# Kernel tuning notes

Hardware: AMD Instinct MI355X
Metric: run time of the kernel (lower is better)

The kernel has to match this reference:

```python
import jax, jax.numpy as jnp
import numpy as np

N_HEADS = 16
LATENT = 16          # latent_vec_len (1D RoPE portion of head_dim)
ROPE_BASE = 10000.0
HIDDEN = 1024


def _rope_1d_tables(seq_len, d):
    m = d // 2
    inv_freq = 1.0 / (ROPE_BASE ** (jnp.arange(m, dtype=jnp.float32) * 2.0 / d))
    ang = jnp.arange(seq_len, dtype=jnp.float32)[:, None] * inv_freq[None, :]  # (S, m)
    return jnp.cos(ang), jnp.sin(ang)


def _rope_2d_tables(height, width, d):
    m = d // 4
    inv_freq = 1.0 / (ROPE_BASE ** (jnp.arange(m, dtype=jnp.float32) * 4.0 / d))
    xa = jnp.arange(width, dtype=jnp.float32)[:, None] * inv_freq[None, :]   # (W, m)
    ya = jnp.arange(height, dtype=jnp.float32)[:, None] * inv_freq[None, :]  # (H, m)
    S = height * width
    cos_x = jnp.broadcast_to(jnp.cos(xa)[None, :, :], (height, width, m)).reshape(S, m)
    sin_x = jnp.broadcast_to(jnp.sin(xa)[None, :, :], (height, width, m)).reshape(S, m)
    cos_y = jnp.broadcast_to(jnp.cos(ya)[:, None, :], (height, width, m)).reshape(S, m)
    sin_y = jnp.broadcast_to(jnp.sin(ya)[:, None, :], (height, width, m)).reshape(S, m)
    return cos_x, sin_x, cos_y, sin_y


def _apply_rope_1d(x, cos, sin):
    # x: (B, n, S, d) with d even; cos/sin: (S, d//2)
    d = x.shape[-1]
    xr = x.reshape(*x.shape[:-1], d // 2, 2)
    a, b = xr[..., 0], xr[..., 1]
    na = a * cos - b * sin
    nb = a * sin + b * cos
    return jnp.stack((na, nb), axis=-1).reshape(x.shape)


def _apply_rope_2d(x, cos_x, sin_x, cos_y, sin_y):
    # x: (B, n, S, d) with d % 4 == 0; tables: (S, d//4)
    q = x.shape[-1] // 4
    xr, xi = x[..., :q], x[..., q:2 * q]
    yr, yi = x[..., 2 * q:3 * q], x[..., 3 * q:]
    return jnp.concatenate([
        xr * cos_x - xi * sin_x,
        xr * sin_x + xi * cos_x,
        yr * cos_y - yi * sin_y,
        yr * sin_y + yi * cos_y,
    ], axis=-1)


def setup_inputs() -> dict:
    key = jax.random.key(0)
    ks = jax.random.split(key, 9)
    B, S, D = 16, 1024, HIDDEN
    s = 1.0 / np.sqrt(D)
    inp = {
        'x': jax.random.normal(ks[0], (B, S, D), dtype=jnp.float32),
        'Wq': jax.random.uniform(ks[1], (D, D), jnp.float32, -s, s),
        'bq': jax.random.uniform(ks[2], (D,), jnp.float32, -s, s),
        'Wk': jax.random.uniform(ks[3], (D, D), jnp.float32, -s, s),
        'bk': jax.random.uniform(ks[4], (D,), jnp.float32, -s, s),
        'Wv': jax.random.uniform(ks[5], (D, D), jnp.float32, -s, s),
        'bv': jax.random.uniform(ks[6], (D,), jnp.float32, -s, s),
        'Wo': jax.random.uniform(ks[7], (D, D), jnp.float32, -s, s),
        'bo': jax.random.uniform(ks[8], (D,), jnp.float32, -s, s),
        'height': 32,
        'width': 32,
    }
    return inp


def reference(x, Wq, bq, Wk, bk, Wv, bv, Wo, bo, height, width):
    B, S, D = x.shape
    n, h = N_HEADS, D // N_HEADS
    spatial = h - LATENT
    scale = 1.0 / np.sqrt(h)

    def heads(t):
        return t.reshape(B, S, n, h).transpose(0, 2, 1, 3)  # (B, n, S, h)

    q = heads(x @ Wq.T + bq)
    k = heads(x @ Wk.T + bk)
    v = heads(x @ Wv.T + bv)

    cos1, sin1 = _rope_1d_tables(S, LATENT)
    cx, sx, cy, sy = _rope_2d_tables(height, width, spatial)

    ql = _apply_rope_1d(q[..., :LATENT], cos1, sin1)
    kl = _apply_rope_1d(k[..., :LATENT], cos1, sin1)
    qs = _apply_rope_2d(q[..., LATENT:], cx, sx, cy, sy)
    ks_ = _apply_rope_2d(k[..., LATENT:], cx, sx, cy, sy)

    qr = jnp.concatenate([ql, qs], axis=-1)
    kr = jnp.concatenate([kl, ks_], axis=-1)

    attn = jax.nn.softmax(jnp.einsum('bnsh,bnth->bnst', qr, kr) * scale, axis=-1)
    out = jnp.einsum('bnst,bnth->bnsh', attn, v)
    out = out.transpose(0, 2, 1, 3).reshape(B, S, D)
    return out @ Wo.T + bo
```

## Files before the change

### kernel.cpp

```cpp
#include <hip/hip_runtime.h>
#include <math.h>

#define B_ 16
#define S_ 1024
#define D_ 1024
#define NH_ 16
#define M_TOT (B_ * S_)

typedef __attribute__((ext_vector_type(8))) short short8v;
typedef __attribute__((ext_vector_type(4))) short short4v;
typedef __attribute__((ext_vector_type(4))) float float4v;
typedef __attribute__((ext_vector_type(4))) unsigned int uint4v;

static __device__ __forceinline__ unsigned short f2bf(float f) {
  union { float f; unsigned u; } x; x.f = f;
  unsigned r = (x.u + 0x7fffu + ((x.u >> 16) & 1u)) >> 16;
  return (unsigned short)r;
}
static __device__ __forceinline__ float bf2f(unsigned short u) {
  union { unsigned u; float f; } x; x.u = ((unsigned)u) << 16;
  return x.f;
}

static __device__ __forceinline__ unsigned pack2bf(float a, float b) {
  return ((unsigned)f2bf(b) << 16) | (unsigned)f2bf(a);
}

static __device__ __forceinline__ void load_lds16(const unsigned short* g, unsigned short* l) {
  __builtin_amdgcn_global_load_lds(
      (const __attribute__((address_space(1))) unsigned int*)g,
      (__attribute__((address_space(3))) unsigned int*)l, 16, 0, 0);
}

__global__ void build_tables(float* __restrict__ cos1, float* __restrict__ sin1,
                             float* __restrict__ cos2, float* __restrict__ sin2) {
  int t = blockIdx.x * 256 + threadIdx.x;
  if (t < S_ * 8) {
    int s = t >> 3, i = t & 7;
    double ang = (double)s * pow(10000.0, -(double)i / 8.0);
    cos1[t] = (float)cos(ang);
    sin1[t] = (float)sin(ang);
  } else if (t < S_ * 8 + 384) {
    int u = t - S_ * 8;
    int p = u / 12, j = u - p * 12;
    double ang = (double)p * pow(10000.0, -(double)j / 12.0);
    cos2[u] = (float)cos(ang);
    sin2[u] = (float)sin(ang);
  }
}

__global__ __launch_bounds__(256) void f32_to_bf16(
    const float* __restrict__ src, unsigned short* __restrict__ dst, int n4) {
  int i = blockIdx.x * 256 + threadIdx.x;
  if (i < n4) {
    float4 v = ((const float4*)src)[i];
    unsigned short t[4] = {f2bf(v.x), f2bf(v.y), f2bf(v.z), f2bf(v.w)};
    ((short4v*)dst)[i] = *(short4v*)t;
  }
}

__global__ __launch_bounds__(256) void w4_to_bf16(
    const float* __restrict__ w0, const float* __restrict__ w1,
    const float* __restrict__ w2, const float* __restrict__ w3,
    unsigned short* __restrict__ dst) {
  const float* srcs[4] = {w0, w1, w2, w3};
  const float* src = srcs[blockIdx.y];
  unsigned short* d = dst + (size_t)blockIdx.y * D_ * D_;
  int i = blockIdx.x * 256 + threadIdx.x;
  float4 v = ((const float4*)src)[i];
  unsigned short t[4] = {f2bf(v.x), f2bf(v.y), f2bf(v.z), f2bf(v.w)};
  ((short4v*)d)[i] = *(short4v*)t;
}

template <bool BF16OUT>
__global__ __launch_bounds__(256) void gemm_mfma(
    const unsigned short* __restrict__ A, const unsigned short* __restrict__ W,
    const float* __restrict__ bias, void* __restrict__ Cout) {
  __shared__ unsigned short As[128 * 32];
  __shared__ unsigned short Bs[128 * 32];
  const int t = threadIdx.x;
  const int w = t >> 6, L = t & 63;
  const int c = L & 15, g = L >> 4;
  const int id = blockIdx.x;
  const int xcd = id & 7, slot = id >> 3;
  const int bn = (slot & 7) * 128;
  const int bm = ((slot >> 3) * 8 + xcd) * 128;

  const int srow = w * 32 + (L >> 2);
  const int sko = (L & 3) * 8;
  const unsigned short* gA = A + (size_t)(bm + srow) * D_ + sko;
  const unsigned short* gB = W + (size_t)(bn + srow) * D_ + sko;
  unsigned short* lA = As + w * 1024;
  unsigned short* lB = Bs + w * 1024;

  const int wm = (w >> 1) * 64, wn = (w & 1) * 64;

  float4v acc[4][4];
#pragma unroll
  for (int i = 0; i < 4; ++i)
#pragma unroll
    for (int j = 0; j < 4; ++j) acc[i][j] = (float4v){0.f, 0.f, 0.f, 0.f};

  for (int k0 = 0; k0 < D_; k0 += 32) {
    __syncthreads();
    load_lds16(gA + k0, lA);
    load_lds16(gA + k0 + 16 * D_, lA + 512);
    load_lds16(gB + k0, lB);
    load_lds16(gB + k0 + 16 * D_, lB + 512);
    __syncthreads();
    short8v af[4], bf[4];
#pragma unroll
    for (int i = 0; i < 4; ++i)
      af[i] = *(const short8v*)&As[(wm + 16 * i + c) * 32 + 8 * g];
#pragma unroll
    for (int j = 0; j < 4; ++j)
      bf[j] = *(const short8v*)&Bs[(wn + 16 * j + c) * 32 + 8 * g];
#pragma unroll
    for (int i = 0; i < 4; ++i)
#pragma unroll
      for (int j = 0; j < 4; ++j)
        acc[i][j] = __builtin_amdgcn_mfma_f32_16x16x32_bf16(af[i], bf[j], acc[i][j], 0, 0, 0);
  }
#pragma unroll
  for (int i = 0; i < 4; ++i)
#pragma unroll
    for (int r = 0; r < 4; ++r) {
      const size_t row = (size_t)bm + wm + 16 * i + 4 * g + r;
#pragma unroll
      for (int j = 0; j < 4; ++j) {
        const int col = bn + wn + 16 * j + c;
        float vv = acc[i][j][r] + bias[col];
        if (BF16OUT)
          ((unsigned short*)Cout)[row * D_ + col] = f2bf(vv);
        else
          ((float*)Cout)[row * D_ + col] = vv;
      }
    }
}

__global__ __launch_bounds__(256) void rope_inplace(
    unsigned short* q,
    const float* __restrict__ cos1, const float* __restrict__ sin1,
    const float* __restrict__ cos2, const float* __restrict__ sin2,
    float scale) {
  int tid = blockIdx.x * 256 + threadIdx.x;
  int u = tid & 511;
  int m = tid >> 9;
  int s = m & (S_ - 1);
  int head = u >> 5, w = u & 31;
  size_t base = (size_t)m * D_ + head * 64;
  size_t c0, c1;
  float cv, sv;
  if (w < 8) {
    c0 = base + 2 * w; c1 = c0 + 1;
    cv = cos1[s * 8 + w]; sv = sin1[s * 8 + w];
  } else if (w < 20) {
    int j = w - 8, x = s & 31;
    c0 = base + 16 + j; c1 = base + 28 + j;
    cv = cos2[x * 12 + j]; sv = sin2[x * 12 + j];
  } else {
    int j = w - 20, y = s >> 5;
    c0 = base + 40 + j; c1 = base + 52 + j;
    cv = cos2[y * 12 + j]; sv = sin2[y * 12 + j];
  }
  float a = bf2f(q[c0]), b = bf2f(q[c1]);
  q[c0] = f2bf((a * cv - b * sv) * scale);
  q[c1] = f2bf((a * sv + b * cv) * scale);
}

__global__ __launch_bounds__(256) void v_transpose(
    const unsigned short* __restrict__ v, unsigned short* __restrict__ vT) {
  __shared__ unsigned short T[64][72];
  const int t = threadIdx.x;
  const int st0 = blockIdx.x * 64;
  const int hd = blockIdx.y, b = blockIdx.z;
  const unsigned short* src = v + ((size_t)b * S_ + st0) * D_ + hd * 64;
#pragma unroll
  for (int rep = 0; rep < 4; ++rep) {
    int id = t + rep * 256;
    int s = id >> 4, n4 = (id & 15) * 4;
    short4v val = *(const short4v*)(src + (size_t)s * D_ + n4);
    T[n4 + 0][s] = val[0]; T[n4 + 1][s] = val[1];
    T[n4 + 2][s] = val[2]; T[n4 + 3][s] = val[3];
  }
  __syncthreads();
  unsigned short* dst = vT + ((size_t)(b * NH_ + hd) * 64) * S_ + st0;
#pragma unroll
  for (int rep = 0; rep < 2; ++rep) {
    int id = t + rep * 256;
    int n = id >> 3, s8 = (id & 7) * 8;
    unsigned short tmp[8];
#pragma unroll
    for (int u2 = 0; u2 < 8; ++u2) tmp[u2] = T[n][s8 + u2];
    *(short8v*)(dst + (size_t)n * S_ + s8) = *(short8v*)tmp;
  }
}

__global__ __launch_bounds__(256, 4) void attn_mfma(
    const unsigned short* __restrict__ qb, const unsigned short* __restrict__ kb,
    const unsigned short* __restrict__ vT, unsigned short* __restrict__ out) {
  __shared__ unsigned short KV[2][2][4096];
  const int t = threadIdx.x;
  const int w = t >> 6;
  const int L = t & 63;
  const int c = L & 15;
  const int g = L >> 4;
  const int id = blockIdx.x;
  const int xcd = id & 7, slot = id >> 3;
  const int qt = slot & 7;
  const int pair = (slot >> 3) * 8 + xcd;
  const int b = pair >> 4, hd = pair & 15;
  const size_t mrow0 = (size_t)b * S_ + qt * 128 + w * 32;
  const int dcol0 = hd * 64;

  const int lrow = L >> 3;
  const int lcol = ((L & 7) ^ lrow) * 8;

  const int a_lo = (((L & 16) ? 32 : 0) + c) * 4;
  const int a_hi = a_lo + 64;
  const bool ghi = (L >= 32);
  const int swz = (c & 7) << 3;

  short8v aq[2][2];
#pragma unroll
  for (int i = 0; i < 2; ++i)
#pragma unroll
    for (int st = 0; st < 2; ++st)
      aq[i][st] = *(const short8v*)(qb + (mrow0 + 16 * i + c) * D_ + dcol0 + 32 * st + 8 * g);

  float4v oacc[2][4];
  float lsum[2] = {0.f, 0.f};
#pragma unroll
  for (int i = 0; i < 2; ++i)
#pragma unroll
    for (int jv = 0; jv < 4; ++jv) oacc[i][jv] = (float4v){0.f, 0.f, 0.f, 0.f};

  const unsigned short* vbase = vT + (size_t)(b * NH_ + hd) * 64 * S_;
  const unsigned short* kbb = kb + (size_t)b * S_ * D_ + dcol0;

#define STAGE(buf, kt_)                                                          \
  {                                                                              \
    _Pragma("unroll")                                                            \
    for (int e = 0; e < 2; ++e) {                                                \
      const int seg = 2 * w + e;                                                 \
      const int row = seg * 8 + lrow;                                            \
      load_lds16(kbb + (size_t)((kt_) * 64 + row) * D_ + lcol,                   \
                 &KV[buf][0][seg * 512]);                                        \
      load_lds16(vbase + (size_t)row * S_ + (kt_) * 64 + lcol,                   \
                 &KV[buf][1][seg * 512]);                                        \
    }                                                                            \
  }

  STAGE(0, 0);
  asm volatile("s_waitcnt vmcnt(0)" ::: "memory");
  __syncthreads();

#pragma unroll 1
  for (int kt = 0; kt < 16; ++kt) {
    const int cur = kt & 1;
    if (kt < 15) STAGE(cur ^ 1, kt + 1);
#pragma unroll
    for (int st = 0; st < 2; ++st) {
      short8v vfh[4];
#pragma unroll
      for (int jv = 0; jv < 4; ++jv)
        vfh[jv] = *(const short8v*)&KV[cur][1][((16 * jv + c) * 64 + st * 32 + 8 * g) ^ swz];
      short8v kfh[2][2];
#pragma unroll
      for (int jl = 0; jl < 2; ++jl)
#pragma unroll
        for (int h = 0; h < 2; ++h)
          kfh[jl][h] = *(const short8v*)&KV[cur][0][((16 * (2 * st + jl) + c) * 64 + h * 32 + 8 * g) ^ swz];
      float4v sacch[2][2];
#pragma unroll
      for (int i = 0; i < 2; ++i)
#pragma unroll
        for (int jl = 0; jl < 2; ++jl) sacch[i][jl] = (float4v){0.f, 0.f, 0.f, 0.f};
      __builtin_amdgcn_s_setprio(1);
#pragma unroll
      for (int jl = 0; jl < 2; ++jl)
#pragma unroll
        for (int i = 0; i < 2; ++i) {
          sacch[i][jl] = __builtin_amdgcn_mfma_f32_16x16x32_bf16(kfh[jl][0], aq[i][0], sacch[i][jl], 0, 0, 0);
          sacch[i][jl] = __builtin_amdgcn_mfma_f32_16x16x32_bf16(kfh[jl][1], aq[i][1], sacch[i][jl], 0, 0, 0);
        }
      __builtin_amdgcn_s_setprio(0);
      unsigned pkh[2][2][2];
#pragma unroll
      for (int i = 0; i < 2; ++i)
#pragma unroll
        for (int jl = 0; jl < 2; ++jl) {
          float p0 = __expf(sacch[i][jl][0]);
          float p1 = __expf(sacch[i][jl][1]);
          float p2 = __expf(sacch[i][jl][2]);
          float p3 = __expf(sacch[i][jl][3]);
          lsum[i] += (p0 + p1) + (p2 + p3);
          pkh[i][jl][0] = pack2bf(p0, p1);
          pkh[i][jl][1] = pack2bf(p2, p3);
        }
      short8v aph[2];
#pragma unroll
      for (int i = 0; i < 2; ++i) {
        uint4v wv;
#pragma unroll
        for (int q2 = 0; q2 < 4; ++q2) {
          const int addr = (q2 & 2) ? a_hi : a_lo;
          int vlo = __builtin_amdgcn_ds_bpermute(addr, (int)pkh[i][0][q2 & 1]);
          int vhi = __builtin_amdgcn_ds_bpermute(addr, (int)pkh[i][1][q2 & 1]);
          wv[q2] = (unsigned)(ghi ? vhi : vlo);
        }
        aph[i] = *(short8v*)&wv;
      }
      __builtin_amdgcn_s_setprio(1);
#pragma unroll
      for (int jv = 0; jv < 4; ++jv)
#pragma unroll
        for (int i = 0; i < 2; ++i)
          oacc[i][jv] = __builtin_amdgcn_mfma_f32_16x16x32_bf16(aph[i], vfh[jv], oacc[i][jv], 0, 0, 0);
      __builtin_amdgcn_s_setprio(0);
    }
    asm volatile("s_waitcnt vmcnt(0)" ::: "memory");
    __syncthreads();
  }
#undef STAGE
#pragma unroll
  for (int i = 0; i < 2; ++i) {
    float ls = lsum[i];
    ls += __shfl_xor(ls, 16);
    ls += __shfl_xor(ls, 32);
#pragma unroll
    for (int r = 0; r < 4; ++r) {
      float inv = 1.f / __shfl(ls, 4 * g + r);
      size_t row = mrow0 + 16 * i + 4 * g + r;
#pragma unroll
      for (int jv = 0; jv < 4; ++jv)
        out[row * D_ + dcol0 + 16 * jv + c] = f2bf(oacc[i][jv][r] * inv);
    }
  }
}

extern "C" void kernel_launch(void* const* d_in, const int* in_sizes, int n_in,
                              void* d_out, int out_size, void* d_ws, size_t ws_size,
                              hipStream_t stream) {
  const float* x  = (const float*)d_in[0];
  const float* Wq = (const float*)d_in[1];
  const float* bq = (const float*)d_in[2];
  const float* Wk = (const float*)d_in[3];
  const float* bk = (const float*)d_in[4];
  const float* Wv = (const float*)d_in[5];
  const float* bv = (const float*)d_in[6];
  const float* Wo = (const float*)d_in[7];
  const float* bo = (const float*)d_in[8];
  float* out = (float*)d_out;

  char* ws = (char*)d_ws;
  const size_t SZ2 = (size_t)M_TOT * D_ * 2;
  unsigned short* xb = (unsigned short*)(ws);
  unsigned short* ob = xb;
  unsigned short* qb = (unsigned short*)(ws + SZ2);
  unsigned short* kb = (unsigned short*)(ws + 2 * SZ2);
  unsigned short* vb = (unsigned short*)(ws + 3 * SZ2);
  unsigned short* vT = (unsigned short*)(ws + 4 * SZ2);
  unsigned short* wqb = (unsigned short*)(ws + 5 * SZ2);
  unsigned short* wkb = wqb + (size_t)D_ * D_;
  unsigned short* wvb = wkb + (size_t)D_ * D_;
  unsigned short* wob = wvb + (size_t)D_ * D_;
  float* cos1 = (float*)(ws + 5 * SZ2 + 4 * (size_t)D_ * D_ * 2);
  float* sin1 = cos1 + S_ * 8;
  float* cos2 = sin1 + S_ * 8;
  float* sin2 = cos2 + 384;

  build_tables<<<34, 256, 0, stream>>>(cos1, sin1, cos2, sin2);

  f32_to_bf16<<<M_TOT * D_ / 4 / 256, 256, 0, stream>>>(x, xb, M_TOT * D_ / 4);
  w4_to_bf16<<<dim3(D_ * D_ / 4 / 256, 4), 256, 0, stream>>>(Wq, Wk, Wv, Wo, wqb);

  gemm_mfma<true><<<1024, 256, 0, stream>>>(xb, wqb, bq, qb);
  gemm_mfma<true><<<1024, 256, 0, stream>>>(xb, wkb, bk, kb);
  gemm_mfma<true><<<1024, 256, 0, stream>>>(xb, wvb, bv, vb);

  const int rope_blocks = (M_TOT * 512) / 256;
  rope_inplace<<<rope_blocks, 256, 0, stream>>>(qb, cos1, sin1, cos2, sin2, 0.125f);
  rope_inplace<<<rope_blocks, 256, 0, stream>>>(kb, cos1, sin1, cos2, sin2, 1.0f);
  v_transpose<<<dim3(16, 16, 16), 256, 0, stream>>>(vb, vT);

  attn_mfma<<<2048, 256, 0, stream>>>(qb, kb, vT, ob);

  gemm_mfma<false><<<1024, 256, 0, stream>>>(ob, wob, bo, out);
}
```

Before: 491.4 us.

## Double-buffer GEMM LDS loads and merge small kernels into fewer launches

The GEMM now double-buffers its LDS tiles, prefetching the next K slice while the current one is fed to MFMA, so the two barriers per iteration become one wait plus one barrier. The Q/K/V projections become a single grid with blockIdx.y selecting the weight, bias and output, relying on qb/kb/vb being contiguous in the workspace. The conversion and table-building kernels are fused into one prep kernel, and the two RoPE passes plus the V transpose are fused into one postproc kernel, cutting launch count and tail effects. Doubling LDS per block may lower occupancy, and the fused kernels still do the same per-element work.

```diff
diff --git a/kernel.cpp b/kernel.cpp
--- a/kernel.cpp
+++ b/kernel.cpp
@@ -32,52 +32,54 @@
       (__attribute__((address_space(3))) unsigned int*)l, 16, 0, 0);
 }
 
-__global__ void build_tables(float* __restrict__ cos1, float* __restrict__ sin1,
-                             float* __restrict__ cos2, float* __restrict__ sin2) {
-  int t = blockIdx.x * 256 + threadIdx.x;
-  if (t < S_ * 8) {
-    int s = t >> 3, i = t & 7;
-    double ang = (double)s * pow(10000.0, -(double)i / 8.0);
-    cos1[t] = (float)cos(ang);
-    sin1[t] = (float)sin(ang);
-  } else if (t < S_ * 8 + 384) {
-    int u = t - S_ * 8;
-    int p = u / 12, j = u - p * 12;
-    double ang = (double)p * pow(10000.0, -(double)j / 12.0);
-    cos2[u] = (float)cos(ang);
-    sin2[u] = (float)sin(ang);
-  }
-}
-
-__global__ __launch_bounds__(256) void f32_to_bf16(
-    const float* __restrict__ src, unsigned short* __restrict__ dst, int n4) {
-  int i = blockIdx.x * 256 + threadIdx.x;
-  if (i < n4) {
-    float4 v = ((const float4*)src)[i];
-    unsigned short t[4] = {f2bf(v.x), f2bf(v.y), f2bf(v.z), f2bf(v.w)};
-    ((short4v*)dst)[i] = *(short4v*)t;
-  }
-}
-
-__global__ __launch_bounds__(256) void w4_to_bf16(
+__global__ __launch_bounds__(256) void prep(
+    const float* __restrict__ x, unsigned short* __restrict__ xb,
     const float* __restrict__ w0, const float* __restrict__ w1,
     const float* __restrict__ w2, const float* __restrict__ w3,
-    unsigned short* __restrict__ dst) {
-  const float* srcs[4] = {w0, w1, w2, w3};
-  const float* src = srcs[blockIdx.y];
-  unsigned short* d = dst + (size_t)blockIdx.y * D_ * D_;
-  int i = blockIdx.x * 256 + threadIdx.x;
-  float4 v = ((const float4*)src)[i];
-  unsigned short t[4] = {f2bf(v.x), f2bf(v.y), f2bf(v.z), f2bf(v.w)};
-  ((short4v*)d)[i] = *(short4v*)t;
+    unsigned short* __restrict__ wdst,
+    float* __restrict__ cos1, float* __restrict__ sin1,
+    float* __restrict__ cos2, float* __restrict__ sin2) {
+  const int bid = blockIdx.x;
+  if (bid < 16384) {
+    int i = bid * 256 + threadIdx.x;
+    float4 v = ((const float4*)x)[i];
+    unsigned short tt[4] = {f2bf(v.x), f2bf(v.y), f2bf(v.z), f2bf(v.w)};
+    ((short4v*)xb)[i] = *(short4v*)tt;
+  } else if (bid < 20480) {
+    int wi = (bid - 16384) * 256 + threadIdx.x;
+    int m = wi >> 18;
+    int i = wi & 262143;
+    const float* src = (m == 0) ? w0 : (m == 1) ? w1 : (m == 2) ? w2 : w3;
+    float4 v = ((const float4*)src)[i];
+    unsigned short tt[4] = {f2bf(v.x), f2bf(v.y), f2bf(v.z), f2bf(v.w)};
+    ((short4v*)(wdst + (size_t)m * D_ * D_))[i] = *(short4v*)tt;
+  } else {
+    int t = (bid - 20480) * 256 + threadIdx.x;
+    if (t < S_ * 8) {
+      int s = t >> 3, i = t & 7;
+      double ang = (double)s * pow(10000.0, -(double)i / 8.0);
+      cos1[t] = (float)cos(ang);
+      sin1[t] = (float)sin(ang);
+    } else if (t < S_ * 8 + 384) {
+      int u = t - S_ * 8;
+      int p = u / 12, j = u - p * 12;
+      double ang = (double)p * pow(10000.0, -(double)j / 12.0);
+      cos2[u] = (float)cos(ang);
+      sin2[u] = (float)sin(ang);
+    }
+  }
 }
 
 template <bool BF16OUT>
 __global__ __launch_bounds__(256) void gemm_mfma(
-    const unsigned short* __restrict__ A, const unsigned short* __restrict__ W,
-    const float* __restrict__ bias, void* __restrict__ Cout) {
-  __shared__ unsigned short As[128 * 32];
-  __shared__ unsigned short Bs[128 * 32];
+    const unsigned short* __restrict__ A, const unsigned short* __restrict__ Wall,
+    const float* __restrict__ b0, const float* __restrict__ b1,
+    const float* __restrict__ b2, void* __restrict__ Cout) {
+  __shared__ unsigned short As[2][128 * 32];
+  __shared__ unsigned short Bs[2][128 * 32];
+  const int y = blockIdx.y;
+  const unsigned short* W = Wall + (size_t)y * D_ * D_;
+  const float* bias = (y == 0) ? b0 : (y == 1) ? b1 : b2;
   const int t = threadIdx.x;
   const int w = t >> 6, L = t & 63;
   const int c = L & 15, g = L >> 4;
@@ -90,8 +92,6 @@
   const int sko = (L & 3) * 8;
   const unsigned short* gA = A + (size_t)(bm + srow) * D_ + sko;
   const unsigned short* gB = W + (size_t)(bn + srow) * D_ + sko;
-  unsigned short* lA = As + w * 1024;
-  unsigned short* lB = Bs + w * 1024;
 
   const int wm = (w >> 1) * 64, wn = (w & 1) * 64;
 
@@ -101,26 +101,38 @@
 #pragma unroll
     for (int j = 0; j < 4; ++j) acc[i][j] = (float4v){0.f, 0.f, 0.f, 0.f};
 
+#define GS(buf, k0_)                                                  \
+  {                                                                   \
+    load_lds16(gA + (k0_), &As[buf][w * 1024]);                       \
+    load_lds16(gA + (k0_) + 16 * D_, &As[buf][w * 1024 + 512]);       \
+    load_lds16(gB + (k0_), &Bs[buf][w * 1024]);                       \
+    load_lds16(gB + (k0_) + 16 * D_, &Bs[buf][w * 1024 + 512]);       \
+  }
+
+  GS(0, 0);
+  asm volatile("s_waitcnt vmcnt(0)" ::: "memory");
+  __syncthreads();
+  int cur = 0;
   for (int k0 = 0; k0 < D_; k0 += 32) {
-    __syncthreads();
-    load_lds16(gA + k0, lA);
-    load_lds16(gA + k0 + 16 * D_, lA + 512);
-    load_lds16(gB + k0, lB);
-    load_lds16(gB + k0 + 16 * D_, lB + 512);
-    __syncthreads();
+    if (k0 + 32 < D_) GS(cur ^ 1, k0 + 32);
     short8v af[4], bf[4];
 #pragma unroll
     for (int i = 0; i < 4; ++i)
-      af[i] = *(const short8v*)&As[(wm + 16 * i + c) * 32 + 8 * g];
+      af[i] = *(const short8v*)&As[cur][(wm + 16 * i + c) * 32 + 8 * g];
 #pragma unroll
     for (int j = 0; j < 4; ++j)
-      bf[j] = *(const short8v*)&Bs[(wn + 16 * j + c) * 32 + 8 * g];
+      bf[j] = *(const short8v*)&Bs[cur][(wn + 16 * j + c) * 32 + 8 * g];
 #pragma unroll
     for (int i = 0; i < 4; ++i)
 #pragma unroll
       for (int j = 0; j < 4; ++j)
         acc[i][j] = __builtin_amdgcn_mfma_f32_16x16x32_bf16(af[i], bf[j], acc[i][j], 0, 0, 0);
-  }
+    asm volatile("s_waitcnt vmcnt(0)" ::: "memory");
+    __syncthreads();
+    cur ^= 1;
+  }
+#undef GS
+  unsigned short* Cb = (unsigned short*)Cout + (size_t)y * M_TOT * D_;
 #pragma unroll
   for (int i = 0; i < 4; ++i)
 #pragma unroll
@@ -131,68 +143,71 @@
         const int col = bn + wn + 16 * j + c;
         float vv = acc[i][j][r] + bias[col];
         if (BF16OUT)
-          ((unsigned short*)Cout)[row * D_ + col] = f2bf(vv);
+          Cb[row * D_ + col] = f2bf(vv);
         else
           ((float*)Cout)[row * D_ + col] = vv;
       }
     }
 }
 
-__global__ __launch_bounds__(256) void rope_inplace(
-    unsigned short* q,
+__global__ __launch_bounds__(256) void postproc(
+    unsigned short* __restrict__ qb, unsigned short* __restrict__ kbuf,
+    const unsigned short* __restrict__ vb, unsigned short* __restrict__ vT,
     const float* __restrict__ cos1, const float* __restrict__ sin1,
-    const float* __restrict__ cos2, const float* __restrict__ sin2,
-    float scale) {
-  int tid = blockIdx.x * 256 + threadIdx.x;
-  int u = tid & 511;
-  int m = tid >> 9;
-  int s = m & (S_ - 1);
-  int head = u >> 5, w = u & 31;
-  size_t base = (size_t)m * D_ + head * 64;
-  size_t c0, c1;
-  float cv, sv;
-  if (w < 8) {
-    c0 = base + 2 * w; c1 = c0 + 1;
-    cv = cos1[s * 8 + w]; sv = sin1[s * 8 + w];
-  } else if (w < 20) {
-    int j = w - 8, x = s & 31;
-    c0 = base + 16 + j; c1 = base + 28 + j;
-    cv = cos2[x * 12 + j]; sv = sin2[x * 12 + j];
+    const float* __restrict__ cos2, const float* __restrict__ sin2) {
+  __shared__ unsigned short T[64][72];
+  const int bid = blockIdx.x;
+  if (bid < 65536) {
+    unsigned short* q = (bid < 32768) ? qb : kbuf;
+    const float scale = (bid < 32768) ? 0.125f : 1.0f;
+    int tid = (bid & 32767) * 256 + threadIdx.x;
+    int u = tid & 511;
+    int m = tid >> 9;
+    int s = m & (S_ - 1);
+    int head = u >> 5, w = u & 31;
+    size_t base = (size_t)m * D_ + head * 64;
+    size_t c0, c1;
+    float cv, sv;
+    if (w < 8) {
+      c0 = base + 2 * w; c1 = c0 + 1;
+      cv = cos1[s * 8 + w]; sv = sin1[s * 8 + w];
+    } else if (w < 20) {
+      int j = w - 8, x = s & 31;
+      c0 = base + 16 + j; c1 = base + 28 + j;
+      cv = cos2[x * 12 + j]; sv = sin2[x * 12 + j];
+    } else {
+      int j = w - 20, yy = s >> 5;
+      c0 = base + 40 + j; c1 = base + 52 + j;
+      cv = cos2[yy * 12 + j]; sv = sin2[yy * 12 + j];
+    }
+    float a = bf2f(q[c0]), b = bf2f(q[c1]);
+    q[c0] = f2bf((a * cv - b * sv) * scale);
+    q[c1] = f2bf((a * sv + b * cv) * scale);
   } else {
-    int j = w - 20, y = s >> 5;
-    c0 = base + 40 + j; c1 = base + 52 + j;
-    cv = cos2[y * 12 + j]; sv = sin2[y * 12 + j];
-  }
-  float a = bf2f(q[c0]), b = bf2f(q[c1]);
-  q[c0] = f2bf((a * cv - b * sv) * scale);
-  q[c1] = f2bf((a * sv + b * cv) * scale);
-}
-
-__global__ __launch_bounds__(256) void v_transpose(
-    const unsigned short* __restrict__ v, unsigned short* __restrict__ vT) {
-  __shared__ unsigned short T[64][72];
-  const int t = threadIdx.x;
-  const int st0 = blockIdx.x * 64;
-  const int hd = blockIdx.y, b = blockIdx.z;
-  const unsigned short* src = v + ((size_t)b * S_ + st0) * D_ + hd * 64;
-#pragma unroll
-  for (int rep = 0; rep < 4; ++rep) {
-    int id = t + rep * 256;
-    int s = id >> 4, n4 = (id & 15) * 4;
-    short4v val = *(const short4v*)(src + (size_t)s * D_ + n4);
-    T[n4 + 0][s] = val[0]; T[n4 + 1][s] = val[1];
-    T[n4 + 2][s] = val[2]; T[n4 + 3][s] = val[3];
-  }
-  __syncthreads();
-  unsigned short* dst = vT + ((size_t)(b * NH_ + hd) * 64) * S_ + st0;
-#pragma unroll
-  for (int rep = 0; rep < 2; ++rep) {
-    int id = t + rep * 256;
-    int n = id >> 3, s8 = (id & 7) * 8;
-    unsigned short tmp[8];
-#pragma unroll
-    for (int u2 = 0; u2 < 8; ++u2) tmp[u2] = T[n][s8 + u2];
-    *(short8v*)(dst + (size_t)n * S_ + s8) = *(short8v*)tmp;
+    const int tb = bid - 65536;
+    const int t = threadIdx.x;
+    const int st0 = (tb & 15) * 64;
+    const int hd = (tb >> 4) & 15, b = tb >> 8;
+    const unsigned short* src = vb + ((size_t)b * S_ + st0) * D_ + hd * 64;
+#pragma unroll
+    for (int rep = 0; rep < 4; ++rep) {
+      int id = t + rep * 256;
+      int s = id >> 4, n4 = (id & 15) * 4;
+      short4v val = *(const short4v*)(src + (size_t)s * D_ + n4);
+      T[n4 + 0][s] = val[0]; T[n4 + 1][s] = val[1];
+      T[n4 + 2][s] = val[2]; T[n4 + 3][s] = val[3];
+    }
+    __syncthreads();
+    unsigned short* dst = vT + ((size_t)(b * NH_ + hd) * 64) * S_ + st0;
+#pragma unroll
+    for (int rep = 0; rep < 2; ++rep) {
+      int id = t + rep * 256;
+      int n = id >> 3, s8 = (id & 7) * 8;
+      unsigned short tmp[8];
+#pragma unroll
+      for (int u2 = 0; u2 < 8; ++u2) tmp[u2] = T[n][s8 + u2];
+      *(short8v*)(dst + (size_t)n * S_ + s8) = *(short8v*)tmp;
+    }
   }
 }
 
@@ -362,29 +377,16 @@
   unsigned short* vb = (unsigned short*)(ws + 3 * SZ2);
   unsigned short* vT = (unsigned short*)(ws + 4 * SZ2);
   unsigned short* wqb = (unsigned short*)(ws + 5 * SZ2);
-  unsigned short* wkb = wqb + (size_t)D_ * D_;
-  unsigned short* wvb = wkb + (size_t)D_ * D_;
-  unsigned short* wob = wvb + (size_t)D_ * D_;
+  unsigned short* wob = wqb + 3 * (size_t)D_ * D_;
   float* cos1 = (float*)(ws + 5 * SZ2 + 4 * (size_t)D_ * D_ * 2);
   float* sin1 = cos1 + S_ * 8;
   float* cos2 = sin1 + S_ * 8;
   float* sin2 = cos2 + 384;
 
-  build_tables<<<34, 256, 0, stream>>>(cos1, sin1, cos2, sin2);
-
-  f32_to_bf16<<<M_TOT * D_ / 4 / 256, 256, 0, stream>>>(x, xb, M_TOT * D_ / 4);
-  w4_to_bf16<<<dim3(D_ * D_ / 4 / 256, 4), 256, 0, stream>>>(Wq, Wk, Wv, Wo, wqb);
-
-  gemm_mfma<true><<<1024, 256, 0, stream>>>(xb, wqb, bq, qb);
-  gemm_mfma<true><<<1024, 256, 0, stream>>>(xb, wkb, bk, kb);
-  gemm_mfma<true><<<1024, 256, 0, stream>>>(xb, wvb, bv, vb);
-
-  const int rope_blocks = (M_TOT * 512) / 256;
-  rope_inplace<<<rope_blocks, 256, 0, stream>>>(qb, cos1, sin1, cos2, sin2, 0.125f);
-  rope_inplace<<<rope_blocks, 256, 0, stream>>>(kb, cos1, sin1, cos2, sin2, 1.0f);
-  v_transpose<<<dim3(16, 16, 16), 256, 0, stream>>>(vb, vT);
-
+  prep<<<20514, 256, 0, stream>>>(x, xb, Wq, Wk, Wv, Wo, wqb,
+                                  cos1, sin1, cos2, sin2);
+  gemm_mfma<true><<<dim3(1024, 3), 256, 0, stream>>>(xb, wqb, bq, bk, bv, qb);
+  postproc<<<69632, 256, 0, stream>>>(qb, kb, vb, vT, cos1, sin1, cos2, sin2);
   attn_mfma<<<2048, 256, 0, stream>>>(qb, kb, vT, ob);
-
-  gemm_mfma<false><<<1024, 256, 0, stream>>>(ob, wob, bo, out);
-}
+  gemm_mfma<false><<<dim3(1024, 1), 256, 0, stream>>>(ob, wob, bo, bo, bo, out);
+}
```

New measurement: 485.4 us. About the same (-1.2%).
